# Kernel optimization log

Hardware: AMD Instinct MI355X
Metric: run time of the kernel (lower is better)

## Reference

```python
import jax, jax.numpy as jnp
import numpy as np

DIM = 1024
INTER = 4096
NUM_EXPERTS = 8
TOP_K = 2
NUM_TOKENS = 8192


def setup_inputs() -> dict:
    key = jax.random.key(0)
    ks = jax.random.split(key, 6)
    scale = 0.02
    return {
        "hidden_states": jax.random.normal(ks[0], (NUM_TOKENS, DIM), dtype=jnp.float32),
        # shared expert (stored as [in, out] so y = x @ W; same math as torch Linear)
        "shared_w1": jax.random.normal(ks[1], (DIM, INTER), dtype=jnp.float32) * scale,
        "shared_w2": jax.random.normal(ks[2], (INTER, DIM), dtype=jnp.float32) * scale,
        # routed experts, stacked: [E, in, out]
        "routed_w1": jax.random.normal(ks[3], (NUM_EXPERTS, DIM, INTER), dtype=jnp.float32) * scale,
        "routed_w2": jax.random.normal(ks[4], (NUM_EXPERTS, INTER, DIM), dtype=jnp.float32) * scale,
        # router: [dim, E]
        "router_w": jax.random.normal(ks[5], (DIM, NUM_EXPERTS), dtype=jnp.float32) * scale,
    }


def reference(hidden_states, shared_w1, shared_w2, routed_w1, routed_w2, router_w):
    # shared expert FFN
    shared_out = jnp.maximum(hidden_states @ shared_w1, 0) @ shared_w2  # [T, D]

    # router -> top-k -> softmax over the selected logits
    router_logits = hidden_states @ router_w                      # [T, E]
    top_vals, top_idx = jax.lax.top_k(router_logits, TOP_K)       # [T, K]
    routing_weights = jax.nn.softmax(top_vals, axis=-1)           # [T, K]

    # per-token combine weight for each expert: [T, E]
    onehot = jax.nn.one_hot(top_idx, NUM_EXPERTS, dtype=hidden_states.dtype)  # [T, K, E]
    combine = jnp.einsum('tk,tke->te', routing_weights, onehot)   # [T, E]

    # dense all-expert FFN (same math as gather/scatter loop, vectorized)
    h = jnp.einsum('td,edf->etf', hidden_states, routed_w1)       # [E, T, F]
    h = jnp.maximum(h, 0)
    expert_out = jnp.einsum('etf,efd->etd', h, routed_w2)         # [E, T, D]
    routed_out = jnp.einsum('etd,te->td', expert_out, combine)    # [T, D]

    return shared_out + routed_out
```

## Files before the change

kernel.cpp:

```cpp
#include <hip/hip_runtime.h>
#include <hip/hip_bf16.h>


#define T_TOKENS 8192
#define DIM      1024
#define INTER    4096
#define NEXP     8

typedef short bf16x8 __attribute__((ext_vector_type(8)));
typedef float f32x4  __attribute__((ext_vector_type(4)));

__device__ __forceinline__ unsigned short f2b(float f) {
  union { float f; unsigned int u; } v; v.f = f;
  unsigned int u = v.u;
  return (unsigned short)((u + 0x7FFFu + ((u >> 16) & 1u)) >> 16);
}

__device__ __forceinline__ void load_lds16(const unsigned short* g, unsigned short* l) {
  __builtin_amdgcn_global_load_lds(
      (const __attribute__((address_space(1))) void*)g,
      (__attribute__((address_space(3))) void*)l, 16, 0, 0);
}

__global__ void cast_x_kernel(const float* __restrict__ x, unsigned short* __restrict__ xb) {
  size_t i = ((size_t)blockIdx.x * 256 + threadIdx.x) * 4;
  float4 v = *(const float4*)(x + i);
  ushort4 o;
  o.x = f2b(v.x); o.y = f2b(v.y); o.z = f2b(v.z); o.w = f2b(v.w);
  *(ushort4*)(xb + i) = o;
}

__global__ void transpose_cast_kernel(const float* __restrict__ routed,
                                      const float* __restrict__ shared_w,
                                      unsigned short* __restrict__ outb,
                                      int K, int N) {
  int e = blockIdx.z;
  const float* in = (e < NEXP) ? routed + (size_t)e * K * N : shared_w;
  unsigned short* out = outb + (size_t)e * K * N;
  __shared__ float tile[32][33];
  int n0 = blockIdx.x * 32, k0 = blockIdx.y * 32;
  int tid = threadIdx.x;
  int c = tid & 31, r0 = tid >> 5;
#pragma unroll
  for (int i = 0; i < 4; i++) {
    int r = r0 + i * 8;
    tile[r][c] = in[(size_t)(k0 + r) * N + n0 + c];
  }
  __syncthreads();
  int rr = tid >> 3;
  int c4 = (tid & 7) * 4;
  ushort4 o;
  o.x = f2b(tile[c4 + 0][rr]); o.y = f2b(tile[c4 + 1][rr]);
  o.z = f2b(tile[c4 + 2][rr]); o.w = f2b(tile[c4 + 3][rr]);
  *(ushort4*)(out + (size_t)(n0 + rr) * K + k0 + c4) = o;
}

__global__ void router_topk_kernel(const float* __restrict__ x, const float* __restrict__ rw,
                                   int* __restrict__ top_idx, float* __restrict__ top_w) {
  int wv = threadIdx.x >> 6, lane = threadIdx.x & 63;
  int t = blockIdx.x * 4 + wv;
  const float* xr = x + (size_t)t * DIM;
  float a[8];
#pragma unroll
  for (int e = 0; e < 8; e++) a[e] = 0.f;
#pragma unroll
  for (int i = 0; i < 16; i++) {
    int d = i * 64 + lane;
    float xv = xr[d];
    float4 r0 = *(const float4*)(rw + d * 8);
    float4 r1 = *(const float4*)(rw + d * 8 + 4);
    a[0] += xv * r0.x; a[1] += xv * r0.y; a[2] += xv * r0.z; a[3] += xv * r0.w;
    a[4] += xv * r1.x; a[5] += xv * r1.y; a[6] += xv * r1.z; a[7] += xv * r1.w;
  }
#pragma unroll
  for (int s = 32; s; s >>= 1) {
#pragma unroll
    for (int e = 0; e < 8; e++) a[e] += __shfl_down(a[e], s);
  }
  if (lane == 0) {
    int be = 0; float bv = a[0];
#pragma unroll
    for (int e = 1; e < 8; e++) if (a[e] > bv) { bv = a[e]; be = e; }
    int be2 = -1; float bv2 = -3.4e38f;
#pragma unroll
    for (int e = 0; e < 8; e++) if (e != be && a[e] > bv2) { bv2 = a[e]; be2 = e; }
    float w0 = 1.f / (1.f + __expf(bv2 - bv));
    top_idx[t] = be | (be2 << 8);
    top_w[t] = w0;
  }
}

__global__ void bucket_kernel(const int* __restrict__ top_idx, const float* __restrict__ top_w,
                              int* __restrict__ counts, int* __restrict__ offs,
                              int* __restrict__ tok_list, float* __restrict__ tok_w) {
  __shared__ int lcount[NEXP];
  int tid = threadIdx.x;
  if (tid < NEXP) lcount[tid] = 0;
  __syncthreads();
  for (int t = tid; t < T_TOKENS; t += 256) {
    int p = top_idx[t];
    float w0 = top_w[t];
    int e0 = p & 0xff, e1 = p >> 8;
    int s0 = atomicAdd(&lcount[e0], 1);
    tok_list[e0 * T_TOKENS + s0] = t; tok_w[e0 * T_TOKENS + s0] = w0;
    int s1 = atomicAdd(&lcount[e1], 1);
    tok_list[e1 * T_TOKENS + s1] = t; tok_w[e1 * T_TOKENS + s1] = 1.f - w0;
  }
  __syncthreads();
  if (tid == 0) {
    int run = 0;
    for (int e = 0; e < NEXP; e++) { counts[e] = lcount[e]; offs[e] = run; run += lcount[e]; }
    offs[NEXP] = run;
  }
}

template <int PHASE>
__global__ __launch_bounds__(256) void gemm_kernel(
    const unsigned short* __restrict__ A, const unsigned short* __restrict__ Wt,
    unsigned short* __restrict__ H, float* __restrict__ Out,
    const int* __restrict__ counts, const int* __restrict__ offs,
    const int* __restrict__ tok_list, const float* __restrict__ tok_w,
    int expert_arg, int accmode) {
  const int Kd = (PHASE == 1) ? DIM : INTER;
  int expert = (expert_arg >= 0) ? expert_arg : (int)blockIdx.z;
  int count = (expert < NEXP) ? counts[expert] : T_TOKENS;
  int m0 = blockIdx.y * 128;
  if (m0 >= count) return;
  int n0 = blockIdx.x * 128;
  int hbase = (expert_arg >= 0) ? 0 : ((expert < NEXP) ? offs[expert] : 2 * T_TOKENS);
  const unsigned short* Bt = Wt + (size_t)expert * (4096 * 1024);

  __shared__ __align__(16) unsigned short As[128 * 64];
  __shared__ __align__(16) unsigned short Bs[128 * 64];

  int tid = threadIdx.x;
  int wv = tid >> 6, lane = tid & 63;
  int lrow = lane >> 3;
  int lcol = ((lane & 7) ^ lrow) * 8;

  const unsigned short* aG[4];
  const unsigned short* bG[4];
  unsigned short* aL[4];
  unsigned short* bL[4];
#pragma unroll
  for (int i = 0; i < 4; i++) {
    int r = wv * 32 + i * 8 + lrow;
    int m = m0 + r;
    int src;
    if (PHASE == 1)
      src = (expert < NEXP) ? ((m < count) ? tok_list[expert * T_TOKENS + m] : 0) : m;
    else
      src = hbase + m;
    aG[i] = A + (size_t)src * Kd + lcol;
    bG[i] = Bt + (size_t)(n0 + r) * Kd + lcol;
    aL[i] = &As[(wv * 32 + i * 8) * 64];
    bL[i] = &Bs[(wv * 32 + i * 8) * 64];
  }

  f32x4 acc[4][4];
#pragma unroll
  for (int mf = 0; mf < 4; mf++)
#pragma unroll
    for (int nf = 0; nf < 4; nf++) acc[mf][nf] = (f32x4)0.f;

  int m_off = (wv & 1) * 64, n_off = (wv >> 1) * 64;
  int l15 = lane & 15, q = lane >> 4;
  int sw = l15 & 7;

  for (int k0 = 0; k0 < Kd; k0 += 64) {
#pragma unroll
    for (int i = 0; i < 4; i++) {
      load_lds16(aG[i], aL[i]);
      load_lds16(bG[i], bL[i]);
      aG[i] += 64; bG[i] += 64;
    }
    __syncthreads();
#pragma unroll
    for (int ks = 0; ks < 2; ks++) {
      int cofs = ((ks * 4 + q) ^ sw) * 8;
      bf16x8 af[4], bfr[4];
#pragma unroll
      for (int mf = 0; mf < 4; mf++)
        af[mf] = *(bf16x8*)&As[(m_off + mf * 16 + l15) * 64 + cofs];
#pragma unroll
      for (int nf = 0; nf < 4; nf++)
        bfr[nf] = *(bf16x8*)&Bs[(n_off + nf * 16 + l15) * 64 + cofs];
#pragma unroll
      for (int mf = 0; mf < 4; mf++)
#pragma unroll
        for (int nf = 0; nf < 4; nf++)
          acc[mf][nf] = __builtin_amdgcn_mfma_f32_16x16x32_bf16(af[mf], bfr[nf], acc[mf][nf], 0, 0, 0);
    }
    __syncthreads();
  }

  if (PHASE == 1) {
#pragma unroll
    for (int mf = 0; mf < 4; mf++)
#pragma unroll
      for (int i = 0; i < 4; i++) {
        int m = m0 + m_off + mf * 16 + q * 4 + i;
        if (m < count) {
#pragma unroll
          for (int nf = 0; nf < 4; nf++) {
            int f = n0 + n_off + nf * 16 + l15;
            float v = acc[mf][nf][i];
            H[(size_t)(hbase + m) * INTER + f] = f2b(v > 0.f ? v : 0.f);
          }
        }
      }
  } else {
#pragma unroll
    for (int mf = 0; mf < 4; mf++)
#pragma unroll
      for (int i = 0; i < 4; i++) {
        int m = m0 + m_off + mf * 16 + q * 4 + i;
        if (m < count) {
          int tokn; float swt;
          if (expert < NEXP) { tokn = tok_list[expert * T_TOKENS + m]; swt = tok_w[expert * T_TOKENS + m]; }
          else { tokn = m; swt = 1.f; }
          float* orow = Out + (size_t)tokn * DIM;
#pragma unroll
          for (int nf = 0; nf < 4; nf++) {
            int d = n0 + n_off + nf * 16 + l15;
            float v = swt * acc[mf][nf][i];
            if (accmode) atomicAdd(orow + d, v);
            else if (expert < NEXP) orow[d] += v;
            else orow[d] = v;
          }
        }
      }
  }
}

extern "C" void kernel_launch(void* const* d_in, const int* in_sizes, int n_in,
                              void* d_out, int out_size, void* d_ws, size_t ws_size,
                              hipStream_t stream) {
  const float* x   = (const float*)d_in[0];
  const float* sw1 = (const float*)d_in[1];
  const float* sw2 = (const float*)d_in[2];
  const float* rw1 = (const float*)d_in[3];
  const float* rw2 = (const float*)d_in[4];
  const float* rtw = (const float*)d_in[5];
  float* out = (float*)d_out;

  char* ws = (char*)d_ws;
  unsigned short* xb  = (unsigned short*)(ws);
  unsigned short* w1t = (unsigned short*)(ws + 16777216);
  unsigned short* w2t = (unsigned short*)(ws + 92274688);
  unsigned short* h   = (unsigned short*)(ws + 167772160);
  int*   top_idx      = (int*)(ws + 167772160);
  float* top_w        = (float*)(ws + 167772160 + 32768);

  const size_t H_BIG  = (size_t)24576 * 4096 * 2;
  const size_t H_SMALL= (size_t)8192  * 4096 * 2;
  const size_t NEED_BIG = 167772160 + H_BIG + 262144 * 2 + 256;
  bool big = ws_size >= NEED_BIG;
  size_t tail = 167772160 + (big ? H_BIG : H_SMALL);
  int*   tok_list = (int*)(ws + tail);
  float* tok_w    = (float*)(ws + tail + 262144);
  int*   counts   = (int*)(ws + tail + 524288);
  int*   offs     = (int*)(ws + tail + 524288 + 64);

  cast_x_kernel<<<(T_TOKENS * DIM) / (256 * 4), 256, 0, stream>>>(x, xb);
  transpose_cast_kernel<<<dim3(128, 32, 9), 256, 0, stream>>>(rw1, sw1, w1t, 1024, 4096);
  transpose_cast_kernel<<<dim3(32, 128, 9), 256, 0, stream>>>(rw2, sw2, w2t, 4096, 1024);
  router_topk_kernel<<<T_TOKENS / 4, 256, 0, stream>>>(x, rtw, top_idx, top_w);
  bucket_kernel<<<1, 256, 0, stream>>>(top_idx, top_w, counts, offs, tok_list, tok_w);

  if (big) {
    hipMemsetAsync(out, 0, (size_t)T_TOKENS * DIM * sizeof(float), stream);
    gemm_kernel<1><<<dim3(32, 64, 9), 256, 0, stream>>>(xb, w1t, h, nullptr,
                                                        counts, offs, tok_list, tok_w, -1, 1);
    gemm_kernel<2><<<dim3(8, 64, 9), 256, 0, stream>>>(h, w2t, nullptr, out,
                                                       counts, offs, tok_list, tok_w, -1, 1);
  } else {
    gemm_kernel<1><<<dim3(32, 64), 256, 0, stream>>>(xb, w1t, h, nullptr,
                                                     counts, offs, tok_list, tok_w, 8, 0);
    gemm_kernel<2><<<dim3(8, 64), 256, 0, stream>>>(h, w2t, nullptr, out,
                                                    counts, offs, tok_list, tok_w, 8, 0);
    for (int e = 0; e < 8; e++) {
      gemm_kernel<1><<<dim3(32, 64), 256, 0, stream>>>(xb, w1t, h, nullptr,
                                                       counts, offs, tok_list, tok_w, e, 0);
      gemm_kernel<2><<<dim3(8, 64), 256, 0, stream>>>(h, w2t, nullptr, out,
                                                      counts, offs, tok_list, tok_w, e, 0);
    }
  }
}
```

Before: 1.083 ms.

## Double-buffer LDS tiles to overlap global loads with MFMA compute

Splits the A and B shared-memory tiles into two buffers and issues the async global-to-LDS loads for the next K tile before computing on the current one. This removes one barrier per iteration and lets memory latency hide behind MFMA work. It doubles LDS use per block (64 KB), which may reduce how many blocks fit on a CU. The single remaining barrier per iteration may not guarantee the async loads have landed, since no explicit vmcnt wait is added.

```diff
diff --git a/kernel.cpp b/kernel.cpp
--- a/kernel.cpp
+++ b/kernel.cpp
@@ -130,8 +130,8 @@
   int hbase = (expert_arg >= 0) ? 0 : ((expert < NEXP) ? offs[expert] : 2 * T_TOKENS);
   const unsigned short* Bt = Wt + (size_t)expert * (4096 * 1024);
 
-  __shared__ __align__(16) unsigned short As[128 * 64];
-  __shared__ __align__(16) unsigned short Bs[128 * 64];
+  __shared__ __align__(16) unsigned short As[2][128 * 64];
+  __shared__ __align__(16) unsigned short Bs[2][128 * 64];
 
   int tid = threadIdx.x;
   int wv = tid >> 6, lane = tid & 63;
@@ -140,8 +140,7 @@
 
   const unsigned short* aG[4];
   const unsigned short* bG[4];
-  unsigned short* aL[4];
-  unsigned short* bL[4];
+  int lofs[4];
 #pragma unroll
   for (int i = 0; i < 4; i++) {
     int r = wv * 32 + i * 8 + lrow;
@@ -153,8 +152,7 @@
       src = hbase + m;
     aG[i] = A + (size_t)src * Kd + lcol;
     bG[i] = Bt + (size_t)(n0 + r) * Kd + lcol;
-    aL[i] = &As[(wv * 32 + i * 8) * 64];
-    bL[i] = &Bs[(wv * 32 + i * 8) * 64];
+    lofs[i] = (wv * 32 + i * 8) * 64;
   }
 
   f32x4 acc[4][4];
@@ -167,32 +165,45 @@
   int l15 = lane & 15, q = lane >> 4;
   int sw = l15 & 7;
 
-  for (int k0 = 0; k0 < Kd; k0 += 64) {
+  auto stage = [&](int buf) {
 #pragma unroll
     for (int i = 0; i < 4; i++) {
-      load_lds16(aG[i], aL[i]);
-      load_lds16(bG[i], bL[i]);
+      load_lds16(aG[i], &As[buf][lofs[i]]);
+      load_lds16(bG[i], &Bs[buf][lofs[i]]);
       aG[i] += 64; bG[i] += 64;
     }
-    __syncthreads();
+  };
+
+  auto compute_tile = [&](int buf) {
 #pragma unroll
     for (int ks = 0; ks < 2; ks++) {
       int cofs = ((ks * 4 + q) ^ sw) * 8;
       bf16x8 af[4], bfr[4];
 #pragma unroll
       for (int mf = 0; mf < 4; mf++)
-        af[mf] = *(bf16x8*)&As[(m_off + mf * 16 + l15) * 64 + cofs];
+        af[mf] = *(bf16x8*)&As[buf][(m_off + mf * 16 + l15) * 64 + cofs];
 #pragma unroll
       for (int nf = 0; nf < 4; nf++)
-        bfr[nf] = *(bf16x8*)&Bs[(n_off + nf * 16 + l15) * 64 + cofs];
+        bfr[nf] = *(bf16x8*)&Bs[buf][(n_off + nf * 16 + l15) * 64 + cofs];
 #pragma unroll
       for (int mf = 0; mf < 4; mf++)
 #pragma unroll
         for (int nf = 0; nf < 4; nf++)
           acc[mf][nf] = __builtin_amdgcn_mfma_f32_16x16x32_bf16(af[mf], bfr[nf], acc[mf][nf], 0, 0, 0);
     }
+  };
+
+  const int nk = Kd / 64;
+  stage(0);
+  __syncthreads();
+  int cur = 0;
+  for (int kt = 0; kt < nk - 1; ++kt) {
+    stage(cur ^ 1);
+    compute_tile(cur);
     __syncthreads();
-  }
+    cur ^= 1;
+  }
+  compute_tile(cur);
 
   if (PHASE == 1) {
 #pragma unroll
```

Result: slower. 1.128 ms (+4.2%).

## Use 256x256 tiles with 4-stage async LDS pipeline and split-K for phase 2

Applied to the files above, without the earlier changes.

Enlarges the GEMM tile to 256x256 with 512 threads, and replaces the single-buffered load/sync loop with a 4-deep ring of 32-wide K slices. The loop waits on vmcnt and a raw barrier so global-to-LDS copies overlap MFMA work, and raises wave priority around the MFMA block. Phase 2 in the batched path is split into two K halves that combine through atomics, to restore parallelism lost to the bigger tiles. The risks are higher register pressure from 32 accumulators per wave, more atomic traffic, and hand-written waitcnt logic that must count outstanding loads exactly.

```diff
diff --git a/kernel.cpp b/kernel.cpp
--- a/kernel.cpp
+++ b/kernel.cpp
@@ -9,6 +9,9 @@
 
 typedef short bf16x8 __attribute__((ext_vector_type(8)));
 typedef float f32x4  __attribute__((ext_vector_type(4)));
+
+#define ASM_VMCNT(n) asm volatile("s_waitcnt vmcnt(" #n ")" ::: "memory")
+#define ASM_BAR()    asm volatile("s_barrier" ::: "memory")
 
 __device__ __forceinline__ unsigned short f2b(float f) {
   union { float f; unsigned int u; } v; v.f = f;
@@ -115,95 +118,118 @@
 }
 
 template <int PHASE>
-__global__ __launch_bounds__(256) void gemm_kernel(
+__global__ __launch_bounds__(512, 2) void gemm_kernel(
     const unsigned short* __restrict__ A, const unsigned short* __restrict__ Wt,
     unsigned short* __restrict__ H, float* __restrict__ Out,
     const int* __restrict__ counts, const int* __restrict__ offs,
     const int* __restrict__ tok_list, const float* __restrict__ tok_w,
     int expert_arg, int accmode) {
   const int Kd = (PHASE == 1) ? DIM : INTER;
-  int expert = (expert_arg >= 0) ? expert_arg : (int)blockIdx.z;
+  int zz = (int)blockIdx.z;
+  int expert, ksp;
+  if (expert_arg >= 0) { expert = expert_arg; ksp = 0; }
+  else if (PHASE == 2) { expert = zz % 9; ksp = zz / 9; }
+  else { expert = zz; ksp = 0; }
+
   int count = (expert < NEXP) ? counts[expert] : T_TOKENS;
-  int m0 = blockIdx.y * 128;
+  int m0 = blockIdx.y * 256;
   if (m0 >= count) return;
-  int n0 = blockIdx.x * 128;
+  int n0 = blockIdx.x * 256;
   int hbase = (expert_arg >= 0) ? 0 : ((expert < NEXP) ? offs[expert] : 2 * T_TOKENS);
   const unsigned short* Bt = Wt + (size_t)expert * (4096 * 1024);
 
-  __shared__ __align__(16) unsigned short As[128 * 64];
-  __shared__ __align__(16) unsigned short Bs[128 * 64];
+  int nt, k0base;
+  if (PHASE == 1) { nt = 32; k0base = 0; }
+  else if (expert_arg >= 0) { nt = 128; k0base = 0; }
+  else { nt = 64; k0base = ksp * 2048; }
+
+  __shared__ __align__(16) unsigned short As[4][256 * 32];
+  __shared__ __align__(16) unsigned short Bs[4][256 * 32];
 
   int tid = threadIdx.x;
   int wv = tid >> 6, lane = tid & 63;
-  int lrow = lane >> 3;
-  int lcol = ((lane & 7) ^ lrow) * 8;
-
-  const unsigned short* aG[4];
-  const unsigned short* bG[4];
-  unsigned short* aL[4];
-  unsigned short* bL[4];
-#pragma unroll
-  for (int i = 0; i < 4; i++) {
-    int r = wv * 32 + i * 8 + lrow;
-    int m = m0 + r;
+  int wv_m = wv >> 2, wv_n = wv & 3;
+  int m_woff = wv_m * 128, n_woff = wv_n * 64;
+
+  int gc = (((lane & 3) ^ ((lane >> 2) & 3)) * 8);
+  const unsigned short* aG[2];
+  const unsigned short* bG[2];
+  int regBase[2];
+#pragma unroll
+  for (int j = 0; j < 2; j++) {
+    int reg = wv * 2 + j;
+    int lr = reg * 16 + (lane >> 2);
     int src;
-    if (PHASE == 1)
+    if (PHASE == 1) {
+      int m = m0 + lr;
       src = (expert < NEXP) ? ((m < count) ? tok_list[expert * T_TOKENS + m] : 0) : m;
-    else
-      src = hbase + m;
-    aG[i] = A + (size_t)src * Kd + lcol;
-    bG[i] = Bt + (size_t)(n0 + r) * Kd + lcol;
-    aL[i] = &As[(wv * 32 + i * 8) * 64];
-    bL[i] = &Bs[(wv * 32 + i * 8) * 64];
-  }
-
-  f32x4 acc[4][4];
-#pragma unroll
-  for (int mf = 0; mf < 4; mf++)
+    } else {
+      src = hbase + m0 + lr;
+    }
+    aG[j] = A + (size_t)src * Kd + k0base + gc;
+    bG[j] = Bt + (size_t)(n0 + lr) * Kd + k0base + gc;
+    regBase[j] = reg * 512;
+  }
+
+  f32x4 acc[8][4];
+#pragma unroll
+  for (int mf = 0; mf < 8; mf++)
 #pragma unroll
     for (int nf = 0; nf < 4; nf++) acc[mf][nf] = (f32x4)0.f;
 
-  int m_off = (wv & 1) * 64, n_off = (wv >> 1) * 64;
   int l15 = lane & 15, q = lane >> 4;
-  int sw = l15 & 7;
-
-  for (int k0 = 0; k0 < Kd; k0 += 64) {
-#pragma unroll
-    for (int i = 0; i < 4; i++) {
-      load_lds16(aG[i], aL[i]);
-      load_lds16(bG[i], bL[i]);
-      aG[i] += 64; bG[i] += 64;
+  int cofs = ((q ^ (l15 & 3)) * 8);
+  int aBase = (m_woff + l15) * 32 + cofs;
+  int bBase = (n_woff + l15) * 32 + cofs;
+
+  auto stage = [&](int buf) {
+#pragma unroll
+    for (int j = 0; j < 2; j++) {
+      load_lds16(aG[j], &As[buf][regBase[j]]);
+      load_lds16(bG[j], &Bs[buf][regBase[j]]);
+      aG[j] += 32; bG[j] += 32;
     }
-    __syncthreads();
-#pragma unroll
-    for (int ks = 0; ks < 2; ks++) {
-      int cofs = ((ks * 4 + q) ^ sw) * 8;
-      bf16x8 af[4], bfr[4];
-#pragma unroll
-      for (int mf = 0; mf < 4; mf++)
-        af[mf] = *(bf16x8*)&As[(m_off + mf * 16 + l15) * 64 + cofs];
+  };
+
+  auto compute_tile = [&](int buf) {
+    const unsigned short* Ab = &As[buf][0];
+    const unsigned short* Bb = &Bs[buf][0];
+    bf16x8 af[8], bfr[4];
+#pragma unroll
+    for (int mf = 0; mf < 8; mf++) af[mf] = *(const bf16x8*)&Ab[aBase + mf * 512];
+#pragma unroll
+    for (int nf = 0; nf < 4; nf++) bfr[nf] = *(const bf16x8*)&Bb[bBase + nf * 512];
+    __builtin_amdgcn_s_setprio(1);
+#pragma unroll
+    for (int mf = 0; mf < 8; mf++)
 #pragma unroll
       for (int nf = 0; nf < 4; nf++)
-        bfr[nf] = *(bf16x8*)&Bs[(n_off + nf * 16 + l15) * 64 + cofs];
-#pragma unroll
-      for (int mf = 0; mf < 4; mf++)
-#pragma unroll
-        for (int nf = 0; nf < 4; nf++)
-          acc[mf][nf] = __builtin_amdgcn_mfma_f32_16x16x32_bf16(af[mf], bfr[nf], acc[mf][nf], 0, 0, 0);
-    }
-    __syncthreads();
-  }
+        acc[mf][nf] = __builtin_amdgcn_mfma_f32_16x16x32_bf16(af[mf], bfr[nf], acc[mf][nf], 0, 0, 0);
+    __builtin_amdgcn_s_setprio(0);
+  };
+
+  stage(0); stage(1); stage(2);
+  ASM_VMCNT(8); ASM_BAR();
+  int t = 0;
+  for (; t + 3 < nt; ++t) {
+    stage((t + 3) & 3);
+    compute_tile(t & 3);
+    ASM_VMCNT(8); ASM_BAR();
+  }
+  compute_tile(t & 3); ASM_VMCNT(4); ASM_BAR(); ++t;
+  compute_tile(t & 3); ASM_VMCNT(0); ASM_BAR(); ++t;
+  compute_tile(t & 3);
 
   if (PHASE == 1) {
 #pragma unroll
-    for (int mf = 0; mf < 4; mf++)
+    for (int mf = 0; mf < 8; mf++)
 #pragma unroll
       for (int i = 0; i < 4; i++) {
-        int m = m0 + m_off + mf * 16 + q * 4 + i;
+        int m = m0 + m_woff + mf * 16 + q * 4 + i;
         if (m < count) {
 #pragma unroll
           for (int nf = 0; nf < 4; nf++) {
-            int f = n0 + n_off + nf * 16 + l15;
+            int f = n0 + n_woff + nf * 16 + l15;
             float v = acc[mf][nf][i];
             H[(size_t)(hbase + m) * INTER + f] = f2b(v > 0.f ? v : 0.f);
           }
@@ -211,10 +237,10 @@
       }
   } else {
 #pragma unroll
-    for (int mf = 0; mf < 4; mf++)
+    for (int mf = 0; mf < 8; mf++)
 #pragma unroll
       for (int i = 0; i < 4; i++) {
-        int m = m0 + m_off + mf * 16 + q * 4 + i;
+        int m = m0 + m_woff + mf * 16 + q * 4 + i;
         if (m < count) {
           int tokn; float swt;
           if (expert < NEXP) { tokn = tok_list[expert * T_TOKENS + m]; swt = tok_w[expert * T_TOKENS + m]; }
@@ -222,7 +248,7 @@
           float* orow = Out + (size_t)tokn * DIM;
 #pragma unroll
           for (int nf = 0; nf < 4; nf++) {
-            int d = n0 + n_off + nf * 16 + l15;
+            int d = n0 + n_woff + nf * 16 + l15;
             float v = swt * acc[mf][nf][i];
             if (accmode) atomicAdd(orow + d, v);
             else if (expert < NEXP) orow[d] += v;
@@ -270,19 +296,19 @@
 
   if (big) {
     hipMemsetAsync(out, 0, (size_t)T_TOKENS * DIM * sizeof(float), stream);
-    gemm_kernel<1><<<dim3(32, 64, 9), 256, 0, stream>>>(xb, w1t, h, nullptr,
+    gemm_kernel<1><<<dim3(16, 32, 9), 512, 0, stream>>>(xb, w1t, h, nullptr,
                                                         counts, offs, tok_list, tok_w, -1, 1);
-    gemm_kernel<2><<<dim3(8, 64, 9), 256, 0, stream>>>(h, w2t, nullptr, out,
-                                                       counts, offs, tok_list, tok_w, -1, 1);
+    gemm_kernel<2><<<dim3(4, 32, 18), 512, 0, stream>>>(h, w2t, nullptr, out,
+                                                        counts, offs, tok_list, tok_w, -1, 1);
   } else {
-    gemm_kernel<1><<<dim3(32, 64), 256, 0, stream>>>(xb, w1t, h, nullptr,
+    gemm_kernel<1><<<dim3(16, 32), 512, 0, stream>>>(xb, w1t, h, nullptr,
                                                      counts, offs, tok_list, tok_w, 8, 0);
-    gemm_kernel<2><<<dim3(8, 64), 256, 0, stream>>>(h, w2t, nullptr, out,
+    gemm_kernel<2><<<dim3(4, 32), 512, 0, stream>>>(h, w2t, nullptr, out,
                                                     counts, offs, tok_list, tok_w, 8, 0);
     for (int e = 0; e < 8; e++) {
-      gemm_kernel<1><<<dim3(32, 64), 256, 0, stream>>>(xb, w1t, h, nullptr,
+      gemm_kernel<1><<<dim3(16, 32), 512, 0, stream>>>(xb, w1t, h, nullptr,
                                                        counts, offs, tok_list, tok_w, e, 0);
-      gemm_kernel<2><<<dim3(8, 64), 256, 0, stream>>>(h, w2t, nullptr, out,
+      gemm_kernel<2><<<dim3(4, 32), 512, 0, stream>>>(h, w2t, nullptr, out,
                                                       counts, offs, tok_list, tok_w, e, 0);
     }
   }
```

Result: slower. 1.211 ms (+11.8%).
